# Kernel tuning notes

Measured on AMD Instinct MI355X. Metric: run time of the kernel, lower is better.

The kernel has to match this reference:

```python
import jax, jax.numpy as jnp
import numpy as np

N_EMBD = 1024
N_HEAD = 16
HEAD_DIM = N_EMBD // N_HEAD


def setup_inputs() -> dict:
    key = jax.random.key(0)
    ks = jax.random.split(key, 9)
    B, S, D = 2, 2048, N_EMBD
    s = 1.0 / np.sqrt(D)
    x = jax.random.normal(ks[0], (B, S, D), dtype=jnp.float32)
    Wq = jax.random.uniform(ks[1], (D, D), jnp.float32, -s, s)
    bq = jax.random.uniform(ks[2], (D,), jnp.float32, -s, s)
    Wk = jax.random.uniform(ks[3], (D, D), jnp.float32, -s, s)
    bk = jax.random.uniform(ks[4], (D,), jnp.float32, -s, s)
    Wv = jax.random.uniform(ks[5], (D, D), jnp.float32, -s, s)
    bv = jax.random.uniform(ks[6], (D,), jnp.float32, -s, s)
    Wp = jax.random.uniform(ks[7], (D, D), jnp.float32, -s, s)
    bp = jax.random.uniform(ks[8], (D,), jnp.float32, -s, s)
    return {"x": x, "Wq": Wq, "bq": bq, "Wk": Wk, "bk": bk,
            "Wv": Wv, "bv": bv, "Wp": Wp, "bp": bp}


def reference(x, Wq, bq, Wk, bk, Wv, bv, Wp, bp):
    B, S, D = x.shape
    H, Hd = N_HEAD, HEAD_DIM
    # Linear layers (torch convention: x @ W.T + b)
    q = (x @ Wq.T + bq).reshape(B, S, H, Hd).transpose(0, 2, 1, 3)  # [B,H,S,Hd]
    k = (x @ Wk.T + bk).reshape(B, S, H, Hd).transpose(0, 2, 1, 3)
    v = (x @ Wv.T + bv).reshape(B, S, H, Hd).transpose(0, 2, 1, 3)
    att = jnp.einsum('bhqd,bhkd->bhqk', q, k) / jnp.sqrt(jnp.float32(Hd))
    causal = jnp.tril(jnp.ones((S, S), dtype=bool))  # [S,S]
    att = jnp.where(causal[None, None], att, -jnp.inf)
    att = jax.nn.softmax(att, axis=-1)
    y = jnp.einsum('bhqk,bhkd->bhqd', att, v)  # [B,H,S,Hd]
    y = y.transpose(0, 2, 1, 3).reshape(B, S, D)
    return y @ Wp.T + bp
```

## Files before the change

kernel.cpp:

```cpp
#include <hip/hip_runtime.h>
#include <hip/hip_bf16.h>

typedef __bf16 bf16;
typedef bf16 bf16x4 __attribute__((ext_vector_type(4)));
typedef bf16 bf16x8 __attribute__((ext_vector_type(8)));
typedef float f32x4 __attribute__((ext_vector_type(4)));
typedef float f32x16 __attribute__((ext_vector_type(16)));
typedef unsigned int u32x4 __attribute__((ext_vector_type(4)));

#define LOG2E 1.44269504088896340736f

__device__ __forceinline__ void gload_lds16(const bf16* g, bf16* l) {
  __builtin_amdgcn_global_load_lds(
      (const __attribute__((address_space(1))) void*)g,
      (__attribute__((address_space(3))) void*)l, 16, 0, 0);
}

__device__ __forceinline__ float fexp2(float x) {
  float r;
  asm("v_exp_f32 %0, %1" : "=v"(r) : "v"(x));
  return r;
}

struct CvtArgs {
  const float* src[5];
  bf16* dst[5];
  int n[5];
};

__global__ __launch_bounds__(256) void cvt_multi(CvtArgs a) {
  const int seg = blockIdx.y;
  const float* __restrict__ s = a.src[seg];
  bf16* __restrict__ d = a.dst[seg];
  const int n = a.n[seg];
  int i = (blockIdx.x * 256 + threadIdx.x) * 4;
  const int stride = gridDim.x * 256 * 4;
  for (; i < n; i += stride) {
    float4 f = *reinterpret_cast<const float4*>(s + i);
    bf16x4 o = {(bf16)f.x, (bf16)f.y, (bf16)f.z, (bf16)f.w};
    *reinterpret_cast<bf16x4*>(d + i) = o;
  }
}

struct GemmBatch {
  const bf16* Bw[3];
  const float* bias[3];
  void* C[3];
};

template <bool OUT_BF16>
__global__ __launch_bounds__(256, 2) void gemm128(const bf16* __restrict__ A,
                                                  GemmBatch gb, int M, int N,
                                                  int K) {
  const int tid = threadIdx.x;
  const int wid = tid >> 6;
  const int lane = tid & 63;
  const int l16 = lane & 15;
  const int hi = lane >> 4;
  const int m0 = blockIdx.x * 128;
  const int n0 = blockIdx.y * 128;
  const int z = blockIdx.z;
  const bf16* __restrict__ Bw = gb.Bw[z];
  const float* __restrict__ bias = gb.bias[z];

  __shared__ bf16 As[128 * 32];
  __shared__ bf16 Bs[128 * 32];

  f32x4 acc[4][4] = {};

  const int wm = (wid >> 1) * 64;
  const int wn = (wid & 1) * 64;

  for (int k0 = 0; k0 < K; k0 += 32) {
#pragma unroll
    for (int i = 0; i < 2; ++i) {
      const int chunk = wid + 4 * i;
      const int p = chunk * 1024 + lane * 16;
      const int row = p >> 6;
      const int cb = (p & 48) ^ ((row & 3) << 4);
      gload_lds16(A + (size_t)(m0 + row) * K + k0 + (cb >> 1), As + chunk * 512);
      gload_lds16(Bw + (size_t)(n0 + row) * K + k0 + (cb >> 1), Bs + chunk * 512);
    }
    __syncthreads();

    bf16x8 af[4], bfr[4];
#pragma unroll
    for (int m = 0; m < 4; ++m) {
      const int r = wm + m * 16 + l16;
      const int pb = r * 64 + ((hi * 16) ^ ((r & 3) << 4));
      af[m] = *reinterpret_cast<const bf16x8*>((const char*)As + pb);
    }
#pragma unroll
    for (int n = 0; n < 4; ++n) {
      const int r = wn + n * 16 + l16;
      const int pb = r * 64 + ((hi * 16) ^ ((r & 3) << 4));
      bfr[n] = *reinterpret_cast<const bf16x8*>((const char*)Bs + pb);
    }
#pragma unroll
    for (int m = 0; m < 4; ++m)
#pragma unroll
      for (int n = 0; n < 4; ++n)
        acc[m][n] =
            __builtin_amdgcn_mfma_f32_16x16x32_bf16(af[m], bfr[n], acc[m][n], 0, 0, 0);
    __syncthreads();
  }

  const int rbase = m0 + wm + hi * 4;
  const int cbase = n0 + wn + l16;
#pragma unroll
  for (int n = 0; n < 4; ++n) {
    const int col = cbase + n * 16;
    const float bv = bias[col];
#pragma unroll
    for (int m = 0; m < 4; ++m) {
#pragma unroll
      for (int j = 0; j < 4; ++j) {
        const int row = rbase + m * 16 + j;
        const float v = acc[m][n][j] + bv;
        if (OUT_BF16)
          ((bf16*)gb.C[z])[(size_t)row * N + col] = (bf16)v;
        else
          ((float*)gb.C[z])[(size_t)row * N + col] = v;
      }
    }
  }
}

__global__ __launch_bounds__(256, 2) void attn_ws(const bf16* __restrict__ Q,
                                                  const bf16* __restrict__ K,
                                                  const bf16* __restrict__ V,
                                                  bf16* __restrict__ Y) {
  const int p = blockIdx.x;
  const int bh = p & 31;
  const int jp = p >> 5;
  const int h = bh & 15;
  const int b = bh >> 4;

  const int tid = threadIdx.x;
  const int w = tid >> 6;
  const int lane = tid & 63;
  const int l31 = lane & 31;
  const int hi2 = lane >> 5;
  const size_t rb = (size_t)b * 2048;
  const int hcol = h * 64;
  const float cl2 = 0.125f * LOG2E;

  __shared__ char smem[20480];
  __shared__ float mlS[4][2][64];
  bf16(*Vt)[40] = (bf16(*)[40])(smem + (size_t)w * 5120);
  float* combf = (float*)smem;

  const int kvg = lane & 7;
  const int dgr = lane >> 3;

  bf16x4 vr0[2][4], vr1[2][4];
  bf16x8 kr0[4], kr1[4];

  auto loadV = [&](bf16x4(&vr)[2][4], int t) {
    const bf16* vp = V + (rb + t * 32 + kvg * 4) * 1024 + hcol + dgr * 4;
#pragma unroll
    for (int r = 0; r < 2; ++r)
#pragma unroll
      for (int jj = 0; jj < 4; ++jj)
        vr[r][jj] = *reinterpret_cast<const bf16x4*>(vp + (size_t)jj * 1024 + r * 32);
  };
  auto loadK = [&](bf16x8(&kr)[4], int t) {
    const bf16* kp = K + (rb + t * 32 + l31) * 1024 + hcol + hi2 * 8;
    kr[0] = *reinterpret_cast<const bf16x8*>(kp);
    kr[1] = *reinterpret_cast<const bf16x8*>(kp + 16);
    kr[2] = *reinterpret_cast<const bf16x8*>(kp + 32);
    kr[3] = *reinterpret_cast<const bf16x8*>(kp + 48);
  };

  auto run = [&](int qg) {
    const int qbase = qg * 64;
    const int NT = 2 * qg + 2;

    bf16x8 qfA[4], qfB[4];
    {
      const bf16* qpA = Q + (rb + qbase + l31) * 1024 + hcol + hi2 * 8;
      const bf16* qpB = qpA + (size_t)32 * 1024;
#pragma unroll
      for (int kt = 0; kt < 4; ++kt) {
        qfA[kt] = *reinterpret_cast<const bf16x8*>(qpA + kt * 16);
        qfB[kt] = *reinterpret_cast<const bf16x8*>(qpB + kt * 16);
      }
    }

    f32x16 yA0 = {}, yA1 = {}, yB0 = {}, yB1 = {};
    float mA = -INFINITY, lA = 0.f, mB = -INFINITY, lB = 0.f;

    auto smax_pv = [&](f32x16& sc, float& m, float& l, f32x16& y0, f32x16& y1) {
      float red[8];
#pragma unroll
      for (int i = 0; i < 8; ++i) red[i] = fmaxf(sc[i], sc[i + 8]);
#pragma unroll
      for (int i = 0; i < 4; ++i) red[i] = fmaxf(red[i], red[i + 4]);
      float pm = fmaxf(fmaxf(red[0], red[1]), fmaxf(red[2], red[3]));
      pm = fmaxf(pm, __shfl_xor(pm, 32));

      if (!__all(pm <= m + 40.f)) {
        const float mn = fmaxf(m, pm);
        const float al = fexp2((m - mn) * cl2);
#pragma unroll
        for (int r = 0; r < 16; ++r) {
          y0[r] *= al;
          y1[r] *= al;
        }
        l *= al;
        m = mn;
      }
      float ps[16];
      const float mc = m * cl2;
#pragma unroll
      for (int r = 0; r < 16; ++r) ps[r] = fexp2(sc[r] * cl2 - mc);
      float sum8[8];
#pragma unroll
      for (int i = 0; i < 8; ++i) sum8[i] = ps[i] + ps[i + 8];
#pragma unroll
      for (int i = 0; i < 4; ++i) sum8[i] += sum8[i + 4];
      float rs = (sum8[0] + sum8[1]) + (sum8[2] + sum8[3]);
      rs += __shfl_xor(rs, 32);
      l += rs;

      unsigned int pk[8];
#pragma unroll
      for (int i = 0; i < 8; ++i) {
        const unsigned short a = __builtin_bit_cast(unsigned short, (bf16)ps[2 * i]);
        const unsigned short c = __builtin_bit_cast(unsigned short, (bf16)ps[2 * i + 1]);
        pk[i] = (unsigned int)a | ((unsigned int)c << 16);
      }
      asm("v_permlane32_swap_b32 %0, %1" : "+v"(pk[0]), "+v"(pk[2]));
      asm("v_permlane32_swap_b32 %0, %1" : "+v"(pk[1]), "+v"(pk[3]));
      asm("v_permlane32_swap_b32 %0, %1" : "+v"(pk[4]), "+v"(pk[6]));
      asm("v_permlane32_swap_b32 %0, %1" : "+v"(pk[5]), "+v"(pk[7]));
      const u32x4 f0 = {pk[0], pk[1], pk[2], pk[3]};
      const u32x4 f1 = {pk[4], pk[5], pk[6], pk[7]};
      const bf16x8 pa0 = __builtin_bit_cast(bf16x8, f0);
      const bf16x8 pa1 = __builtin_bit_cast(bf16x8, f1);

      const bf16x8 va00 = *reinterpret_cast<const bf16x8*>(&Vt[l31][hi2 * 8]);
      const bf16x8 va10 = *reinterpret_cast<const bf16x8*>(&Vt[32 + l31][hi2 * 8]);
      y0 = __builtin_amdgcn_mfma_f32_32x32x16_bf16(va00, pa0, y0, 0, 0, 0);
      y1 = __builtin_amdgcn_mfma_f32_32x32x16_bf16(va10, pa0, y1, 0, 0, 0);
      const bf16x8 va01 = *reinterpret_cast<const bf16x8*>(&Vt[l31][16 + hi2 * 8]);
      const bf16x8 va11 = *reinterpret_cast<const bf16x8*>(&Vt[32 + l31][16 + hi2 * 8]);
      y0 = __builtin_amdgcn_mfma_f32_32x32x16_bf16(va01, pa1, y0, 0, 0, 0);
      y1 = __builtin_amdgcn_mfma_f32_32x32x16_bf16(va11, pa1, y1, 0, 0, 0);
    };

    auto process = [&](bf16x4(&vr)[2][4], bf16x8(&kr)[4], int t) {
#pragma unroll
      for (int r = 0; r < 2; ++r)
#pragma unroll
        for (int kc = 0; kc < 4; ++kc) {
          bf16x4 wv = {vr[r][0][kc], vr[r][1][kc], vr[r][2][kc], vr[r][3][kc]};
          *reinterpret_cast<bf16x4*>(&Vt[r * 32 + dgr * 4 + kc][kvg * 4]) = wv;
        }
      const bool doA = (t != 2 * qg + 1);

      f32x16 scA = {};
      if (doA) {
        scA = __builtin_amdgcn_mfma_f32_32x32x16_bf16(kr[0], qfA[0], scA, 0, 0, 0);
        scA = __builtin_amdgcn_mfma_f32_32x32x16_bf16(kr[1], qfA[1], scA, 0, 0, 0);
        scA = __builtin_amdgcn_mfma_f32_32x32x16_bf16(kr[2], qfA[2], scA, 0, 0, 0);
        scA = __builtin_amdgcn_mfma_f32_32x32x16_bf16(kr[3], qfA[3], scA, 0, 0, 0);
      }
      f32x16 scB = {};
      scB = __builtin_amdgcn_mfma_f32_32x32x16_bf16(kr[0], qfB[0], scB, 0, 0, 0);
      scB = __builtin_amdgcn_mfma_f32_32x32x16_bf16(kr[1], qfB[1], scB, 0, 0, 0);
      scB = __builtin_amdgcn_mfma_f32_32x32x16_bf16(kr[2], qfB[2], scB, 0, 0, 0);
      scB = __builtin_amdgcn_mfma_f32_32x32x16_bf16(kr[3], qfB[3], scB, 0, 0, 0);

      if (t == 2 * qg) {
#pragma unroll
        for (int r = 0; r < 16; ++r) {
          const int kvl = (r & 3) + 8 * (r >> 2) + 4 * hi2;
          if (kvl > l31) scA[r] = -INFINITY;
        }
      }
      if (t == 2 * qg + 1) {
#pragma unroll
        for (int r = 0; r < 16; ++r) {
          const int kvl = (r & 3) + 8 * (r >> 2) + 4 * hi2;
          if (kvl > l31) scB[r] = -INFINITY;
        }
      }

      if (doA) smax_pv(scA, mA, lA, yA0, yA1);
      smax_pv(scB, mB, lB, yB0, yB1);
    };

    int t = w;
    if (t < NT) {
      loadV(vr0, t);
      loadK(kr0, t);
      while (true) {
        int tn = t + 4;
        if (tn < NT) {
          loadV(vr1, tn);
          loadK(kr1, tn);
          __builtin_amdgcn_sched_barrier(0);
        }
        process(vr0, kr0, t);
        t = tn;
        if (t >= NT) break;
        tn = t + 4;
        if (tn < NT) {
          loadV(vr0, tn);
          loadK(kr0, tn);
          __builtin_amdgcn_sched_barrier(0);
        }
        process(vr1, kr1, t);
        t = tn;
        if (t >= NT) break;
      }
    }

    __syncthreads();
    if (lane < 32) {
      mlS[w][0][l31] = mA;
      mlS[w][1][l31] = lA;
      mlS[w][0][32 + l31] = mB;
      mlS[w][1][32 + l31] = lB;
    }

    auto comb_phase = [&](const f32x16& y, int qoff, int dcol) {
#pragma unroll
      for (int r = 0; r < 16; r += 2) {
        const int d0 = (r & 3) + 8 * (r >> 2) + 4 * hi2;
        float2 v2;
        v2.x = y[r];
        v2.y = y[r + 1];
        *reinterpret_cast<float2*>(&combf[((size_t)w * 32 + l31) * 34 + d0]) = v2;
      }
      __syncthreads();

      const int tq = tid >> 3;
      const int dg = (tid & 7) * 4;
      float mw[4], lw[4];
#pragma unroll
      for (int ww = 0; ww < 4; ++ww) {
        mw[ww] = mlS[ww][0][qoff + tq];
        lw[ww] = mlS[ww][1][qoff + tq];
      }
      const float M = fmaxf(fmaxf(mw[0], mw[1]), fmaxf(mw[2], mw[3]));
      float wg[4];
      float Lsum = 0.f;
#pragma unroll
      for (int ww = 0; ww < 4; ++ww) {
        wg[ww] = fexp2((mw[ww] - M) * cl2);
        Lsum += lw[ww] * wg[ww];
      }
      const float inv = 1.f / Lsum;
      float a4[4] = {};
#pragma unroll
      for (int ww = 0; ww < 4; ++ww)
#pragma unroll
        for (int jj = 0; jj < 4; ++jj)
          a4[jj] += wg[ww] * combf[((size_t)ww * 32 + tq) * 34 + dg + jj];
      bf16x4 o;
#pragma unroll
      for (int jj = 0; jj < 4; ++jj) o[jj] = (bf16)(a4[jj] * inv);
      *reinterpret_cast<bf16x4*>(Y + (rb + qbase + qoff + tq) * 1024 + hcol + dcol + dg) = o;
      __syncthreads();
    };

    comb_phase(yA0, 0, 0);
    comb_phase(yA1, 0, 32);
    comb_phase(yB0, 32, 0);
    comb_phase(yB1, 32, 32);
  };

  run(31 - jp);
  run(jp);
}

extern "C" void kernel_launch(void* const* d_in, const int* in_sizes, int n_in,
                              void* d_out, int out_size, void* d_ws,
                              size_t ws_size, hipStream_t stream) {
  const float* x = (const float*)d_in[0];
  const float* Wq = (const float*)d_in[1];
  const float* bq = (const float*)d_in[2];
  const float* Wk = (const float*)d_in[3];
  const float* bk = (const float*)d_in[4];
  const float* Wv = (const float*)d_in[5];
  const float* bv = (const float*)d_in[6];
  const float* Wp = (const float*)d_in[7];
  const float* bp = (const float*)d_in[8];

  const int BS = 4096;
  const int Dm = 1024;

  char* ws = (char*)d_ws;
  bf16* xb = (bf16*)(ws);
  bf16* wqb = (bf16*)(ws + (size_t)(8 << 20));
  bf16* wkb = (bf16*)(ws + (size_t)(10 << 20));
  bf16* wvb = (bf16*)(ws + (size_t)(12 << 20));
  bf16* wpb = (bf16*)(ws + (size_t)(14 << 20));
  bf16* Qb = (bf16*)(ws + (size_t)(16 << 20));
  bf16* Kb = (bf16*)(ws + (size_t)(24 << 20));
  bf16* Vb = (bf16*)(ws + (size_t)(32 << 20));
  bf16* Yb = (bf16*)(ws + (size_t)(40 << 20));

  CvtArgs ca;
  ca.src[0] = x;  ca.dst[0] = xb;  ca.n[0] = BS * Dm;
  ca.src[1] = Wq; ca.dst[1] = wqb; ca.n[1] = Dm * Dm;
  ca.src[2] = Wk; ca.dst[2] = wkb; ca.n[2] = Dm * Dm;
  ca.src[3] = Wv; ca.dst[3] = wvb; ca.n[3] = Dm * Dm;
  ca.src[4] = Wp; ca.dst[4] = wpb; ca.n[4] = Dm * Dm;
  cvt_multi<<<dim3(1024, 5), 256, 0, stream>>>(ca);

  GemmBatch gq;
  gq.Bw[0] = wqb; gq.bias[0] = bq; gq.C[0] = Qb;
  gq.Bw[1] = wkb; gq.bias[1] = bk; gq.C[1] = Kb;
  gq.Bw[2] = wvb; gq.bias[2] = bv; gq.C[2] = Vb;
  gemm128<true><<<dim3(32, 8, 3), 256, 0, stream>>>(xb, gq, BS, Dm, Dm);

  attn_ws<<<dim3(512), 256, 0, stream>>>(Qb, Kb, Vb, Yb);

  GemmBatch gp;
  gp.Bw[0] = wpb; gp.bias[0] = bp; gp.C[0] = d_out;
  gp.Bw[1] = wpb; gp.bias[1] = bp; gp.C[1] = d_out;
  gp.Bw[2] = wpb; gp.bias[2] = bp; gp.C[2] = d_out;
  gemm128<false><<<dim3(32, 8, 1), 256, 0, stream>>>(Yb, gp, BS, Dm, Dm);
}
```

Before: 128.5 us.

## Process 64-key tiles per wave and drop register double-buffered prefetch

Each wave now handles 64 KV rows per iteration instead of 32, so one online-softmax rescale and max/sum reduction covers twice as many scores and there are half as many loop trips. The V transpose into LDS is widened to 64 columns, which raises shared memory per block. The explicit register double-buffering of K/V loads is removed, so global load latency is no longer hidden by prefetching the next tile and may stall. Work per wave also gets coarser, which can worsen load balance across the 4 waves for short causal rows.

```diff
diff --git a/kernel.cpp b/kernel.cpp
--- a/kernel.cpp
+++ b/kernel.cpp
@@ -145,36 +145,38 @@
   const int hcol = h * 64;
   const float cl2 = 0.125f * LOG2E;
 
-  __shared__ char smem[20480];
+  __shared__ char smem[36864];
   __shared__ float mlS[4][2][64];
-  bf16(*Vt)[40] = (bf16(*)[40])(smem + (size_t)w * 5120);
+  bf16(*Vt)[72] = (bf16(*)[72])(smem + (size_t)w * 9216);
   float* combf = (float*)smem;
 
   const int kvg = lane & 7;
   const int dgr = lane >> 3;
 
-  bf16x4 vr0[2][4], vr1[2][4];
-  bf16x8 kr0[4], kr1[4];
-
-  auto loadV = [&](bf16x4(&vr)[2][4], int t) {
-    const bf16* vp = V + (rb + t * 32 + kvg * 4) * 1024 + hcol + dgr * 4;
-#pragma unroll
-    for (int r = 0; r < 2; ++r)
-#pragma unroll
-      for (int jj = 0; jj < 4; ++jj)
-        vr[r][jj] = *reinterpret_cast<const bf16x4*>(vp + (size_t)jj * 1024 + r * 32);
-  };
-  auto loadK = [&](bf16x8(&kr)[4], int t) {
-    const bf16* kp = K + (rb + t * 32 + l31) * 1024 + hcol + hi2 * 8;
-    kr[0] = *reinterpret_cast<const bf16x8*>(kp);
-    kr[1] = *reinterpret_cast<const bf16x8*>(kp + 16);
-    kr[2] = *reinterpret_cast<const bf16x8*>(kp + 32);
-    kr[3] = *reinterpret_cast<const bf16x8*>(kp + 48);
+  auto stageV = [&](int tt) {
+    const bf16* vp0 = V + (rb + tt * 64 + kvg * 4) * 1024 + hcol + dgr * 4;
+#pragma unroll
+    for (int hh = 0; hh < 2; ++hh) {
+      const bf16* vp = vp0 + (size_t)hh * 32 * 1024;
+      bf16x4 vr[2][4];
+#pragma unroll
+      for (int r = 0; r < 2; ++r)
+#pragma unroll
+        for (int jj = 0; jj < 4; ++jj)
+          vr[r][jj] = *reinterpret_cast<const bf16x4*>(vp + (size_t)jj * 1024 + r * 32);
+#pragma unroll
+      for (int r = 0; r < 2; ++r)
+#pragma unroll
+        for (int kc = 0; kc < 4; ++kc) {
+          bf16x4 wv = {vr[r][0][kc], vr[r][1][kc], vr[r][2][kc], vr[r][3][kc]};
+          *reinterpret_cast<bf16x4*>(&Vt[r * 32 + dgr * 4 + kc][hh * 32 + kvg * 4]) = wv;
+        }
+    }
   };
 
   auto run = [&](int qg) {
     const int qbase = qg * 64;
-    const int NT = 2 * qg + 2;
+    const int NT = qg + 1;
 
     bf16x8 qfA[4], qfB[4];
     {
@@ -190,10 +192,12 @@
     f32x16 yA0 = {}, yA1 = {}, yB0 = {}, yB1 = {};
     float mA = -INFINITY, lA = 0.f, mB = -INFINITY, lB = 0.f;
 
-    auto smax_pv = [&](f32x16& sc, float& m, float& l, f32x16& y0, f32x16& y1) {
+    auto smax_pv64 = [&](f32x16& s0, f32x16& s1, float& m, float& l,
+                         f32x16& y0, f32x16& y1, bool skipHi) {
       float red[8];
 #pragma unroll
-      for (int i = 0; i < 8; ++i) red[i] = fmaxf(sc[i], sc[i + 8]);
+      for (int i = 0; i < 8; ++i)
+        red[i] = fmaxf(fmaxf(s0[i], s0[i + 8]), fmaxf(s1[i], s1[i + 8]));
 #pragma unroll
       for (int i = 0; i < 4; ++i) red[i] = fmaxf(red[i], red[i + 4]);
       float pm = fmaxf(fmaxf(red[0], red[1]), fmaxf(red[2], red[3]));
@@ -210,22 +214,26 @@
         l *= al;
         m = mn;
       }
-      float ps[16];
       const float mc = m * cl2;
-#pragma unroll
-      for (int r = 0; r < 16; ++r) ps[r] = fexp2(sc[r] * cl2 - mc);
-      float sum8[8];
-#pragma unroll
-      for (int i = 0; i < 8; ++i) sum8[i] = ps[i] + ps[i + 8];
-#pragma unroll
-      for (int i = 0; i < 4; ++i) sum8[i] += sum8[i + 4];
-      float rs = (sum8[0] + sum8[1]) + (sum8[2] + sum8[3]);
+      float ps[32];
+#pragma unroll
+      for (int r = 0; r < 16; ++r) ps[r] = fexp2(s0[r] * cl2 - mc);
+#pragma unroll
+      for (int r = 0; r < 16; ++r) ps[16 + r] = fexp2(s1[r] * cl2 - mc);
+      float sum[16];
+#pragma unroll
+      for (int i = 0; i < 16; ++i) sum[i] = ps[i] + ps[i + 16];
+#pragma unroll
+      for (int i = 0; i < 8; ++i) sum[i] += sum[i + 8];
+#pragma unroll
+      for (int i = 0; i < 4; ++i) sum[i] += sum[i + 4];
+      float rs = (sum[0] + sum[1]) + (sum[2] + sum[3]);
       rs += __shfl_xor(rs, 32);
       l += rs;
 
-      unsigned int pk[8];
-#pragma unroll
-      for (int i = 0; i < 8; ++i) {
+      unsigned int pk[16];
+#pragma unroll
+      for (int i = 0; i < 16; ++i) {
         const unsigned short a = __builtin_bit_cast(unsigned short, (bf16)ps[2 * i]);
         const unsigned short c = __builtin_bit_cast(unsigned short, (bf16)ps[2 * i + 1]);
         pk[i] = (unsigned int)a | ((unsigned int)c << 16);
@@ -234,87 +242,81 @@
       asm("v_permlane32_swap_b32 %0, %1" : "+v"(pk[1]), "+v"(pk[3]));
       asm("v_permlane32_swap_b32 %0, %1" : "+v"(pk[4]), "+v"(pk[6]));
       asm("v_permlane32_swap_b32 %0, %1" : "+v"(pk[5]), "+v"(pk[7]));
+      asm("v_permlane32_swap_b32 %0, %1" : "+v"(pk[8]), "+v"(pk[10]));
+      asm("v_permlane32_swap_b32 %0, %1" : "+v"(pk[9]), "+v"(pk[11]));
+      asm("v_permlane32_swap_b32 %0, %1" : "+v"(pk[12]), "+v"(pk[14]));
+      asm("v_permlane32_swap_b32 %0, %1" : "+v"(pk[13]), "+v"(pk[15]));
       const u32x4 f0 = {pk[0], pk[1], pk[2], pk[3]};
       const u32x4 f1 = {pk[4], pk[5], pk[6], pk[7]};
+      const u32x4 f2 = {pk[8], pk[9], pk[10], pk[11]};
+      const u32x4 f3 = {pk[12], pk[13], pk[14], pk[15]};
       const bf16x8 pa0 = __builtin_bit_cast(bf16x8, f0);
       const bf16x8 pa1 = __builtin_bit_cast(bf16x8, f1);
-
-      const bf16x8 va00 = *reinterpret_cast<const bf16x8*>(&Vt[l31][hi2 * 8]);
-      const bf16x8 va10 = *reinterpret_cast<const bf16x8*>(&Vt[32 + l31][hi2 * 8]);
-      y0 = __builtin_amdgcn_mfma_f32_32x32x16_bf16(va00, pa0, y0, 0, 0, 0);
-      y1 = __builtin_amdgcn_mfma_f32_32x32x16_bf16(va10, pa0, y1, 0, 0, 0);
-      const bf16x8 va01 = *reinterpret_cast<const bf16x8*>(&Vt[l31][16 + hi2 * 8]);
-      const bf16x8 va11 = *reinterpret_cast<const bf16x8*>(&Vt[32 + l31][16 + hi2 * 8]);
-      y0 = __builtin_amdgcn_mfma_f32_32x32x16_bf16(va01, pa1, y0, 0, 0, 0);
-      y1 = __builtin_amdgcn_mfma_f32_32x32x16_bf16(va11, pa1, y1, 0, 0, 0);
+      const bf16x8 pa2 = __builtin_bit_cast(bf16x8, f2);
+      const bf16x8 pa3 = __builtin_bit_cast(bf16x8, f3);
+
+#pragma unroll
+      for (int ks = 0; ks < 4; ++ks) {
+        if (!(skipHi && ks >= 2)) {
+          const bf16x8 pa = (ks == 0) ? pa0 : (ks == 1) ? pa1 : (ks == 2) ? pa2 : pa3;
+          const bf16x8 va0 = *reinterpret_cast<const bf16x8*>(&Vt[l31][ks * 16 + hi2 * 8]);
+          const bf16x8 va1 = *reinterpret_cast<const bf16x8*>(&Vt[32 + l31][ks * 16 + hi2 * 8]);
+          y0 = __builtin_amdgcn_mfma_f32_32x32x16_bf16(va0, pa, y0, 0, 0, 0);
+          y1 = __builtin_amdgcn_mfma_f32_32x32x16_bf16(va1, pa, y1, 0, 0, 0);
+        }
+      }
     };
 
-    auto process = [&](bf16x4(&vr)[2][4], bf16x8(&kr)[4], int t) {
-#pragma unroll
-      for (int r = 0; r < 2; ++r)
-#pragma unroll
-        for (int kc = 0; kc < 4; ++kc) {
-          bf16x4 wv = {vr[r][0][kc], vr[r][1][kc], vr[r][2][kc], vr[r][3][kc]};
-          *reinterpret_cast<bf16x4*>(&Vt[r * 32 + dgr * 4 + kc][kvg * 4]) = wv;
+    for (int tt = w; tt < NT; tt += 4) {
+      stageV(tt);
+      bf16x8 kr[8];
+      {
+        const bf16* kp = K + (rb + tt * 64 + l31) * 1024 + hcol + hi2 * 8;
+        const bf16* kp2 = kp + (size_t)32 * 1024;
+#pragma unroll
+        for (int i = 0; i < 4; ++i) {
+          kr[i] = *reinterpret_cast<const bf16x8*>(kp + i * 16);
+          kr[4 + i] = *reinterpret_cast<const bf16x8*>(kp2 + i * 16);
         }
-      const bool doA = (t != 2 * qg + 1);
-
-      f32x16 scA = {};
-      if (doA) {
-        scA = __builtin_amdgcn_mfma_f32_32x32x16_bf16(kr[0], qfA[0], scA, 0, 0, 0);
-        scA = __builtin_amdgcn_mfma_f32_32x32x16_bf16(kr[1], qfA[1], scA, 0, 0, 0);
-        scA = __builtin_amdgcn_mfma_f32_32x32x16_bf16(kr[2], qfA[2], scA, 0, 0, 0);
-        scA = __builtin_amdgcn_mfma_f32_32x32x16_bf16(kr[3], qfA[3], scA, 0, 0, 0);
-      }
-      f32x16 scB = {};
-      scB = __builtin_amdgcn_mfma_f32_32x32x16_bf16(kr[0], qfB[0], scB, 0, 0, 0);
-      scB = __builtin_amdgcn_mfma_f32_32x32x16_bf16(kr[1], qfB[1], scB, 0, 0, 0);
-      scB = __builtin_amdgcn_mfma_f32_32x32x16_bf16(kr[2], qfB[2], scB, 0, 0, 0);
-      scB = __builtin_amdgcn_mfma_f32_32x32x16_bf16(kr[3], qfB[3], scB, 0, 0, 0);
-
-      if (t == 2 * qg) {
+      }
+      const bool diag = (tt == qg);
+
+      f32x16 sA0 = {}, sA1, sB0 = {}, sB1 = {};
+      sA0 = __builtin_amdgcn_mfma_f32_32x32x16_bf16(kr[0], qfA[0], sA0, 0, 0, 0);
+      sA0 = __builtin_amdgcn_mfma_f32_32x32x16_bf16(kr[1], qfA[1], sA0, 0, 0, 0);
+      sA0 = __builtin_amdgcn_mfma_f32_32x32x16_bf16(kr[2], qfA[2], sA0, 0, 0, 0);
+      sA0 = __builtin_amdgcn_mfma_f32_32x32x16_bf16(kr[3], qfA[3], sA0, 0, 0, 0);
+      if (!diag) {
+        f32x16 t0 = {};
+        t0 = __builtin_amdgcn_mfma_f32_32x32x16_bf16(kr[4], qfA[0], t0, 0, 0, 0);
+        t0 = __builtin_amdgcn_mfma_f32_32x32x16_bf16(kr[5], qfA[1], t0, 0, 0, 0);
+        t0 = __builtin_amdgcn_mfma_f32_32x32x16_bf16(kr[6], qfA[2], t0, 0, 0, 0);
+        t0 = __builtin_amdgcn_mfma_f32_32x32x16_bf16(kr[7], qfA[3], t0, 0, 0, 0);
+        sA1 = t0;
+      } else {
+#pragma unroll
+        for (int r = 0; r < 16; ++r) sA1[r] = -INFINITY;
+      }
+      sB0 = __builtin_amdgcn_mfma_f32_32x32x16_bf16(kr[0], qfB[0], sB0, 0, 0, 0);
+      sB0 = __builtin_amdgcn_mfma_f32_32x32x16_bf16(kr[1], qfB[1], sB0, 0, 0, 0);
+      sB0 = __builtin_amdgcn_mfma_f32_32x32x16_bf16(kr[2], qfB[2], sB0, 0, 0, 0);
+      sB0 = __builtin_amdgcn_mfma_f32_32x32x16_bf16(kr[3], qfB[3], sB0, 0, 0, 0);
+      sB1 = __builtin_amdgcn_mfma_f32_32x32x16_bf16(kr[4], qfB[0], sB1, 0, 0, 0);
+      sB1 = __builtin_amdgcn_mfma_f32_32x32x16_bf16(kr[5], qfB[1], sB1, 0, 0, 0);
+      sB1 = __builtin_amdgcn_mfma_f32_32x32x16_bf16(kr[6], qfB[2], sB1, 0, 0, 0);
+      sB1 = __builtin_amdgcn_mfma_f32_32x32x16_bf16(kr[7], qfB[3], sB1, 0, 0, 0);
+
+      if (diag) {
 #pragma unroll
         for (int r = 0; r < 16; ++r) {
           const int kvl = (r & 3) + 8 * (r >> 2) + 4 * hi2;
-          if (kvl > l31) scA[r] = -INFINITY;
+          if (kvl > l31) sA0[r] = -INFINITY;
+          if (kvl > l31) sB1[r] = -INFINITY;
         }
       }
-      if (t == 2 * qg + 1) {
-#pragma unroll
-        for (int r = 0; r < 16; ++r) {
-          const int kvl = (r & 3) + 8 * (r >> 2) + 4 * hi2;
-          if (kvl > l31) scB[r] = -INFINITY;
-        }
-      }
-
-      if (doA) smax_pv(scA, mA, lA, yA0, yA1);
-      smax_pv(scB, mB, lB, yB0, yB1);
-    };
-
-    int t = w;
-    if (t < NT) {
-      loadV(vr0, t);
-      loadK(kr0, t);
-      while (true) {
-        int tn = t + 4;
-        if (tn < NT) {
-          loadV(vr1, tn);
-          loadK(kr1, tn);
-          __builtin_amdgcn_sched_barrier(0);
-        }
-        process(vr0, kr0, t);
-        t = tn;
-        if (t >= NT) break;
-        tn = t + 4;
-        if (tn < NT) {
-          loadV(vr0, tn);
-          loadK(kr0, tn);
-          __builtin_amdgcn_sched_barrier(0);
-        }
-        process(vr1, kr1, t);
-        t = tn;
-        if (t >= NT) break;
-      }
+
+      smax_pv64(sA0, sA1, mA, lA, yA0, yA1, diag);
+      smax_pv64(sB0, sB1, mB, lB, yB0, yB1, false);
     }
 
     __syncthreads();
```

Result: no change. 127.9 us (-0.5%).
